# Performance work log

Measured on AMD Instinct MI355X. Metric: run time of the kernel, lower is better.

Reference implementation:

```python
import jax, jax.numpy as jnp
import numpy as np

BS, N, D_IN = 2, 512, 256
HEADS, D_OUT = 8, 64
NEG_SLOPE = 0.2
MASK_VAL = -1000000000.0


def _xavier(key, shape):
    fan_in, fan_out = shape[0], shape[-1]
    limit = float(np.sqrt(6.0 / (fan_in + fan_out)))
    return jax.random.uniform(key, shape, jnp.float32, -limit, limit)


def setup_inputs() -> dict:
    key = jax.random.key(0)
    ks = jax.random.split(key, 6)
    x = jax.random.normal(ks[0], (BS, N, D_IN), jnp.float32)
    adj = jax.random.randint(ks[1], (BS, N, N), 0, 2, jnp.int32)
    # guarantee no fully-masked row (self loops)
    adj = jnp.maximum(adj, jnp.eye(N, dtype=jnp.int32)[None])
    W_src = _xavier(ks[2], (D_IN, HEADS * D_OUT))
    W_tgt = _xavier(ks[3], (D_IN, HEADS * D_OUT))
    W_skip = _xavier(ks[4], (D_IN, HEADS * D_OUT))
    scoring_fn = _xavier(ks[5], (HEADS, D_OUT))
    bias = jnp.zeros((HEADS * D_OUT,), jnp.float32)
    return {"in_nodes_features": x, "adj": adj, "W_src": W_src,
            "W_tgt": W_tgt, "W_skip": W_skip,
            "scoring_fn": scoring_fn, "bias": bias}


def reference(in_nodes_features, adj, W_src, W_tgt, W_skip, scoring_fn, bias):
    x = in_nodes_features
    bs, n, _ = x.shape
    H, d = scoring_fn.shape
    # projections (dropout is identity in eval mode)
    src = (x @ W_src).reshape(bs, n, H, d)  # values & source scores
    tgt = (x @ W_tgt).reshape(bs, n, H, d)
    src_h = jnp.transpose(src, (0, 2, 1, 3))  # (bs,H,n,d)
    tgt_h = jnp.transpose(tgt, (0, 2, 1, 3))  # (bs,H,m,d)
    # GATv2: LeakyReLU(src_i + tgt_j) then dot with scoring vector
    e = jax.nn.leaky_relu(src_h[:, :, :, None, :] + tgt_h[:, :, None, :, :],
                          NEG_SLOPE)              # (bs,H,n,m,d)
    scores = jnp.einsum('hd,bhnmd->bhnm', scoring_fn, e)
    mask = jnp.where(adj[:, None] > 0, 0.0, MASK_VAL)  # (bs,1,n,m)
    attn = jax.nn.softmax(scores + mask, axis=-1)      # (bs,H,n,m)
    out = jnp.einsum('bhnm,bhmd->bhnd', attn, src_h)
    out = jnp.transpose(out, (0, 2, 1, 3))             # (bs,n,H,d)
    # skip connection via skip_proj (dims differ), concat heads, bias, ELU
    out = out + (x @ W_skip).reshape(bs, n, H, d)
    out = out.reshape(bs, n, H * d) + bias
    out = jax.nn.elu(out)
    return out, adj
```

## Files before the change

### kernel.cpp

```cpp
#include <hip/hip_runtime.h>
#include <cstddef>

typedef _Float16 f16;
typedef __attribute__((ext_vector_type(2))) _Float16 f16x2;
typedef __attribute__((ext_vector_type(4))) _Float16 f16x4;
typedef __attribute__((ext_vector_type(8))) _Float16 f16x8;
typedef __attribute__((ext_vector_type(4))) float fx4;

union f16x8u { f16x8 v; f16x2 h[4]; };

#define BS   2
#define NPTS 512
#define DIN  256
#define NH   8
#define DH   64
#define HD   512

__global__ __launch_bounds__(256) void prep_kernel(
    const float* __restrict__ x, const float* __restrict__ W0,
    const float* __restrict__ W1, const float* __restrict__ W2,
    const float* __restrict__ a, const int* __restrict__ adj,
    f16* __restrict__ x16, f16* __restrict__ Wt16, f16* __restrict__ a16,
    float* __restrict__ out_adj)
{
    const int blk = blockIdx.x;
    const int t = threadIdx.x;
    if (blk < 256) {
        int idx = blk * 1024 + t * 4;
        float4 v = *(const float4*)(x + idx);
        f16x4 h = {(f16)v.x, (f16)v.y, (f16)v.z, (f16)v.w};
        *(f16x4*)(x16 + idx) = h;
    } else if (blk < 352) {
        __shared__ float lds[64][65];
        int idx = blk - 256;
        int w = idx >> 5;
        int tile = idx & 31;
        int k0 = (tile >> 3) * 64, n0 = (tile & 7) * 64;
        const float* W = (w == 0) ? W0 : ((w == 1) ? W1 : W2);
        int r = t >> 2;
        int cg = (t & 3) * 16;
        #pragma unroll
        for (int i = 0; i < 4; ++i) {
            float4 v = *(const float4*)(W + (size_t)(k0 + r) * HD + n0 + cg + i * 4);
            lds[r][cg + i * 4 + 0] = v.x;
            lds[r][cg + i * 4 + 1] = v.y;
            lds[r][cg + i * 4 + 2] = v.z;
            lds[r][cg + i * 4 + 3] = v.w;
        }
        __syncthreads();
        f16* dst = Wt16 + (size_t)w * (HD * DIN) + (size_t)(n0 + r) * DIN + k0 + cg;
        #pragma unroll
        for (int i = 0; i < 16; ++i) dst[i] = (f16)lds[cg + i][r];
    } else if (blk == 352) {
        for (int i = t; i < NH * DH; i += 256) a16[i] = (f16)a[i];
    } else {
        int idx = (blk - 353) * 1024 + t * 4;
        int4 v = *(const int4*)(adj + idx);
        float4 fv = {(float)v.x, (float)v.y, (float)v.z, (float)v.w};
        *(float4*)(out_adj + idx) = fv;
    }
}

__global__ __launch_bounds__(256) void proj_kernel(
    const f16* __restrict__ x16, const f16* __restrict__ Wt16,
    f16* __restrict__ src16, f16* __restrict__ srcT16, f16* __restrict__ tgt16,
    float* __restrict__ skipf)
{
    __shared__ f16 Alds[64 * 136];
    __shared__ f16 Blds[64 * 136];
    const int t = threadIdx.x;
    const int mt = blockIdx.x, nt = blockIdx.y, wz = blockIdx.z;
    const f16* Wt = Wt16 + (size_t)wz * (HD * DIN);
    const int lane = t & 63, wv = t >> 6;
    const int l15 = lane & 15, quad = lane >> 4;
    const int moff = (wv & 1) * 32, noff = (wv >> 1) * 32;

    fx4 acc[2][2];
    #pragma unroll
    for (int fi = 0; fi < 2; ++fi)
        #pragma unroll
        for (int fj = 0; fj < 2; ++fj)
            acc[fi][fj] = (fx4){0.f, 0.f, 0.f, 0.f};

    for (int kk = 0; kk < 2; ++kk) {
        if (kk) __syncthreads();
        #pragma unroll
        for (int i = 0; i < 4; ++i) {
            int idx = t + i * 256;
            int row = idx >> 4, seg = idx & 15;
            *(f16x8*)&Alds[row * 136 + seg * 8] =
                *(const f16x8*)(x16 + (size_t)(mt * 64 + row) * DIN + kk * 128 + seg * 8);
            *(f16x8*)&Blds[row * 136 + seg * 8] =
                *(const f16x8*)(Wt + (size_t)(nt * 64 + row) * DIN + kk * 128 + seg * 8);
        }
        __syncthreads();
        #pragma unroll
        for (int ks = 0; ks < 4; ++ks) {
            f16x8 aF[2], bF[2];
            #pragma unroll
            for (int f = 0; f < 2; ++f) {
                aF[f] = *(const f16x8*)&Alds[(moff + f * 16 + l15) * 136 + ks * 32 + quad * 8];
                bF[f] = *(const f16x8*)&Blds[(noff + f * 16 + l15) * 136 + ks * 32 + quad * 8];
            }
            #pragma unroll
            for (int fi = 0; fi < 2; ++fi)
                #pragma unroll
                for (int fj = 0; fj < 2; ++fj)
                    acc[fi][fj] = __builtin_amdgcn_mfma_f32_16x16x32_f16(
                        aF[fi], bF[fj], acc[fi][fj], 0, 0, 0);
        }
    }

    #pragma unroll
    for (int fi = 0; fi < 2; ++fi)
        #pragma unroll
        for (int fj = 0; fj < 2; ++fj)
            #pragma unroll
            for (int i = 0; i < 4; ++i) {
                int rowg = mt * 64 + moff + fi * 16 + quad * 4 + i;
                int colg = nt * 64 + noff + fj * 16 + l15;
                float v = acc[fi][fj][i];
                if (wz == 2) {
                    skipf[(size_t)rowg * HD + colg] = v;
                } else {
                    int bb = rowg >> 9, n = rowg & 511;
                    int hh = colg >> 6, d = colg & 63;
                    size_t bh = (size_t)bb * NH + hh;
                    if (wz == 0) {
                        src16[(bh * NPTS + n) * DH + d] = (f16)v;
                        srcT16[(bh * DH + d) * NPTS + n] = (f16)v;
                    } else {
                        tgt16[(bh * NPTS + n) * DH + d] = (f16)v;
                    }
                }
            }
}

__global__ __launch_bounds__(256) void attn_kernel(
    const f16* __restrict__ src16, const f16* __restrict__ srcT16,
    const f16* __restrict__ tgt16, const f16* __restrict__ a16,
    const float* __restrict__ skipf, const float* __restrict__ bias,
    const int* __restrict__ adj, float* __restrict__ out)
{
    __shared__ f16 tgt_lds[256 * 72];
    __shared__ f16 p_lds[16 * 520];
    __shared__ f16 src_lds[16 * 64];
    __shared__ f16 a_lds[64];

    const int t = threadIdx.x;
    const int lane = t & 63, wv = t >> 6;
    const int n0 = blockIdx.x * 16;
    const int h = blockIdx.y, b = blockIdx.z;
    const int bh = b * NH + h;
    const f16x2 slope2 = {(f16)0.2f, (f16)0.2f};

    if (t < 128) {
        int row = t >> 3, seg = t & 7;
        *(f16x8*)&src_lds[row * 64 + seg * 8] =
            *(const f16x8*)(src16 + ((size_t)bh * NPTS + n0 + row) * DH + seg * 8);
    } else if (t < 136) {
        int seg = t - 128;
        *(f16x8*)&a_lds[seg * 8] = *(const f16x8*)(a16 + h * DH + seg * 8);
    }

    const int r0 = n0 + wv * 4;

    for (int mtile = 0; mtile < 2; ++mtile) {
        __syncthreads();
        #pragma unroll
        for (int i = 0; i < 8; ++i) {
            int idx = t + i * 256;
            int row = idx >> 3, seg = idx & 7;
            *(f16x8*)&tgt_lds[row * 72 + seg * 8] =
                *(const f16x8*)(tgt16 + ((size_t)bh * NPTS + mtile * 256 + row) * DH + seg * 8);
        }
        __syncthreads();

        float sc[4][4] = {{0.f, 0.f, 0.f, 0.f}, {0.f, 0.f, 0.f, 0.f},
                          {0.f, 0.f, 0.f, 0.f}, {0.f, 0.f, 0.f, 0.f}};
        for (int st = 0; st < 8; ++st) {
            f16x8u a8; a8.v = *(const f16x8*)&a_lds[st * 8];
            f16x8u s8[4];
            #pragma unroll
            for (int r = 0; r < 4; ++r)
                s8[r].v = *(const f16x8*)&src_lds[(wv * 4 + r) * 64 + st * 8];
            #pragma unroll
            for (int jj = 0; jj < 4; ++jj) {
                int ml = jj * 64 + lane;
                f16x8u t8; t8.v = *(const f16x8*)&tgt_lds[ml * 72 + st * 8];
                #pragma unroll
                for (int c = 0; c < 4; ++c) {
                    f16x2 t2 = t8.h[c];
                    f16x2 a2 = a8.h[c];
                    #pragma unroll
                    for (int r = 0; r < 4; ++r) {
                        f16x2 z = s8[r].h[c] + t2;
                        f16x2 zl = __builtin_elementwise_max(z, z * slope2);
                        sc[r][jj] = __builtin_amdgcn_fdot2(a2, zl, sc[r][jj], false);
                    }
                }
            }
        }
        #pragma unroll
        for (int r = 0; r < 4; ++r) {
            #pragma unroll
            for (int jj = 0; jj < 4; ++jj) {
                int m = mtile * 256 + jj * 64 + lane;
                int av = adj[((size_t)b * NPTS + r0 + r) * NPTS + m];
                float s = (av > 0) ? sc[r][jj] : -1e30f;
                p_lds[(wv * 4 + r) * 520 + m] = (f16)s;
            }
        }
    }
    __syncthreads();

    #pragma unroll
    for (int r = 0; r < 4; ++r) {
        int row = wv * 4 + r;
        f16x8 v = *(const f16x8*)&p_lds[row * 520 + lane * 8];
        float vf[8];
        #pragma unroll
        for (int i = 0; i < 8; ++i) vf[i] = (float)v[i];
        float mx = vf[0];
        #pragma unroll
        for (int i = 1; i < 8; ++i) mx = fmaxf(mx, vf[i]);
        for (int msk = 1; msk < 64; msk <<= 1) mx = fmaxf(mx, __shfl_xor(mx, msk, 64));
        float l = 0.f;
        #pragma unroll
        for (int i = 0; i < 8; ++i) { vf[i] = __expf(vf[i] - mx); l += vf[i]; }
        for (int msk = 1; msk < 64; msk <<= 1) l += __shfl_xor(l, msk, 64);
        float inv = 1.0f / l;
        f16x8 pv;
        #pragma unroll
        for (int i = 0; i < 8; ++i) pv[i] = (f16)(vf[i] * inv);
        *(f16x8*)&p_lds[row * 520 + lane * 8] = pv;
    }
    __syncthreads();

    const int l15 = lane & 15, quad = lane >> 4;
    fx4 acc = {0.f, 0.f, 0.f, 0.f};
    const f16* vb = srcT16 + ((size_t)bh * DH + wv * 16 + l15) * NPTS;
    #pragma unroll
    for (int ks = 0; ks < 16; ++ks) {
        f16x8 a8 = *(const f16x8*)&p_lds[l15 * 520 + ks * 32 + quad * 8];
        f16x8 b8 = *(const f16x8*)(vb + ks * 32 + quad * 8);
        acc = __builtin_amdgcn_mfma_f32_16x16x32_f16(a8, b8, acc, 0, 0, 0);
    }
    #pragma unroll
    for (int i = 0; i < 4; ++i) {
        int ng = n0 + quad * 4 + i;
        int col = h * DH + wv * 16 + l15;
        size_t oi = ((size_t)b * NPTS + ng) * HD + col;
        float val = acc[i] + skipf[oi] + bias[col];
        out[oi] = (val > 0.f) ? val : __expf(val) - 1.f;
    }
}

extern "C" void kernel_launch(void* const* d_in, const int* in_sizes, int n_in,
                              void* d_out, int out_size, void* d_ws, size_t ws_size,
                              hipStream_t stream) {
    const float* x     = (const float*)d_in[0];
    const int*   adj   = (const int*)d_in[1];
    const float* Wsrc  = (const float*)d_in[2];
    const float* Wtgt  = (const float*)d_in[3];
    const float* Wskip = (const float*)d_in[4];
    const float* a     = (const float*)d_in[5];
    const float* bias  = (const float*)d_in[6];

    float* out = (float*)d_out;
    float* out_adj = out + (size_t)BS * NPTS * NPTS;

    char* wsb = (char*)d_ws;
    f16*   src16  = (f16*)(wsb + 0x000000);
    f16*   srcT16 = (f16*)(wsb + 0x100000);
    f16*   tgt16  = (f16*)(wsb + 0x200000);
    f16*   x16    = (f16*)(wsb + 0x300000);
    f16*   Wt16   = (f16*)(wsb + 0x380000);
    f16*   a16    = (f16*)(wsb + 0x440000);
    float* skipf  = (float*)(wsb + 0x480000);

    prep_kernel<<<865, 256, 0, stream>>>(x, Wsrc, Wtgt, Wskip, a, adj,
                                         x16, Wt16, a16, out_adj);
    proj_kernel<<<dim3(16, 8, 3), 256, 0, stream>>>(x16, Wt16, src16, srcT16,
                                                    tgt16, skipf);
    attn_kernel<<<dim3(32, 8, 2), 256, 0, stream>>>(src16, srcT16, tgt16, a16,
                                                    skipf, bias, adj, out);
}
```

Measured before the change: 103.6 us.

## Fuse fp32-to-fp16 prep into projection GEMM and drop prep kernel launch

Removes the separate prep kernel. The projection kernel now reads fp32 x and W directly, converts them to fp16 while staging into LDS, and transposes W in LDS with scalar stores. The adj-to-float copy moves to extra blocks of the projection kernel, and the attention kernel converts the scoring vector itself. This saves one launch and an intermediate global round trip. In exchange, every GEMM tile re-converts its inputs, and the transposed B writes to LDS may cause bank conflicts.

```diff
diff --git a/kernel.cpp b/kernel.cpp
--- a/kernel.cpp
+++ b/kernel.cpp
@@ -16,63 +16,34 @@
 #define DH   64
 #define HD   512
 
-__global__ __launch_bounds__(256) void prep_kernel(
+__global__ __launch_bounds__(256) void proj_kernel(
     const float* __restrict__ x, const float* __restrict__ W0,
     const float* __restrict__ W1, const float* __restrict__ W2,
-    const float* __restrict__ a, const int* __restrict__ adj,
-    f16* __restrict__ x16, f16* __restrict__ Wt16, f16* __restrict__ a16,
-    float* __restrict__ out_adj)
-{
-    const int blk = blockIdx.x;
-    const int t = threadIdx.x;
-    if (blk < 256) {
-        int idx = blk * 1024 + t * 4;
-        float4 v = *(const float4*)(x + idx);
-        f16x4 h = {(f16)v.x, (f16)v.y, (f16)v.z, (f16)v.w};
-        *(f16x4*)(x16 + idx) = h;
-    } else if (blk < 352) {
-        __shared__ float lds[64][65];
-        int idx = blk - 256;
-        int w = idx >> 5;
-        int tile = idx & 31;
-        int k0 = (tile >> 3) * 64, n0 = (tile & 7) * 64;
-        const float* W = (w == 0) ? W0 : ((w == 1) ? W1 : W2);
-        int r = t >> 2;
-        int cg = (t & 3) * 16;
-        #pragma unroll
-        for (int i = 0; i < 4; ++i) {
-            float4 v = *(const float4*)(W + (size_t)(k0 + r) * HD + n0 + cg + i * 4);
-            lds[r][cg + i * 4 + 0] = v.x;
-            lds[r][cg + i * 4 + 1] = v.y;
-            lds[r][cg + i * 4 + 2] = v.z;
-            lds[r][cg + i * 4 + 3] = v.w;
-        }
-        __syncthreads();
-        f16* dst = Wt16 + (size_t)w * (HD * DIN) + (size_t)(n0 + r) * DIN + k0 + cg;
-        #pragma unroll
-        for (int i = 0; i < 16; ++i) dst[i] = (f16)lds[cg + i][r];
-    } else if (blk == 352) {
-        for (int i = t; i < NH * DH; i += 256) a16[i] = (f16)a[i];
-    } else {
-        int idx = (blk - 353) * 1024 + t * 4;
-        int4 v = *(const int4*)(adj + idx);
-        float4 fv = {(float)v.x, (float)v.y, (float)v.z, (float)v.w};
-        *(float4*)(out_adj + idx) = fv;
-    }
-}
-
-__global__ __launch_bounds__(256) void proj_kernel(
-    const f16* __restrict__ x16, const f16* __restrict__ Wt16,
+    const int* __restrict__ adj,
     f16* __restrict__ src16, f16* __restrict__ srcT16, f16* __restrict__ tgt16,
-    float* __restrict__ skipf)
+    float* __restrict__ skipf, float* __restrict__ out_adj)
 {
     __shared__ f16 Alds[64 * 136];
     __shared__ f16 Blds[64 * 136];
+    const int blk = blockIdx.x;
     const int t = threadIdx.x;
-    const int mt = blockIdx.x, nt = blockIdx.y, wz = blockIdx.z;
-    const f16* Wt = Wt16 + (size_t)wz * (HD * DIN);
     const int lane = t & 63, wv = t >> 6;
     const int l15 = lane & 15, quad = lane >> 4;
+
+    if (blk >= 384) {
+        int id = blk - 384;
+        #pragma unroll
+        for (int j = 0; j < 4; ++j) {
+            int idx = id * 4096 + (t + j * 256) * 4;
+            int4 v = *(const int4*)(adj + idx);
+            float4 fv = {(float)v.x, (float)v.y, (float)v.z, (float)v.w};
+            *(float4*)(out_adj + idx) = fv;
+        }
+        return;
+    }
+
+    const int mt = blk & 15, nt = (blk >> 4) & 7, wz = blk >> 7;
+    const float* W = (wz == 0) ? W0 : ((wz == 1) ? W1 : W2);
     const int moff = (wv & 1) * 32, noff = (wv >> 1) * 32;
 
     fx4 acc[2][2];
@@ -85,13 +56,24 @@
     for (int kk = 0; kk < 2; ++kk) {
         if (kk) __syncthreads();
         #pragma unroll
-        for (int i = 0; i < 4; ++i) {
+        for (int i = 0; i < 8; ++i) {
             int idx = t + i * 256;
-            int row = idx >> 4, seg = idx & 15;
-            *(f16x8*)&Alds[row * 136 + seg * 8] =
-                *(const f16x8*)(x16 + (size_t)(mt * 64 + row) * DIN + kk * 128 + seg * 8);
-            *(f16x8*)&Blds[row * 136 + seg * 8] =
-                *(const f16x8*)(Wt + (size_t)(nt * 64 + row) * DIN + kk * 128 + seg * 8);
+            int row = idx >> 5, c = idx & 31;
+            float4 v = *(const float4*)(x + (size_t)(mt * 64 + row) * DIN
+                                          + kk * 128 + c * 4);
+            f16x4 h = {(f16)v.x, (f16)v.y, (f16)v.z, (f16)v.w};
+            *(f16x4*)&Alds[row * 136 + c * 4] = h;
+        }
+        #pragma unroll
+        for (int i = 0; i < 8; ++i) {
+            int idx = t + i * 256;
+            int k = idx >> 4, c = idx & 15;
+            float4 v = *(const float4*)(W + (size_t)(kk * 128 + k) * HD
+                                          + nt * 64 + c * 4);
+            Blds[(c * 4 + 0) * 136 + k] = (f16)v.x;
+            Blds[(c * 4 + 1) * 136 + k] = (f16)v.y;
+            Blds[(c * 4 + 2) * 136 + k] = (f16)v.z;
+            Blds[(c * 4 + 3) * 136 + k] = (f16)v.w;
         }
         __syncthreads();
         #pragma unroll
@@ -99,8 +81,10 @@
             f16x8 aF[2], bF[2];
             #pragma unroll
             for (int f = 0; f < 2; ++f) {
-                aF[f] = *(const f16x8*)&Alds[(moff + f * 16 + l15) * 136 + ks * 32 + quad * 8];
-                bF[f] = *(const f16x8*)&Blds[(noff + f * 16 + l15) * 136 + ks * 32 + quad * 8];
+                aF[f] = *(const f16x8*)&Alds[(moff + f * 16 + l15) * 136
+                                             + ks * 32 + quad * 8];
+                bF[f] = *(const f16x8*)&Blds[(noff + f * 16 + l15) * 136
+                                             + ks * 32 + quad * 8];
             }
             #pragma unroll
             for (int fi = 0; fi < 2; ++fi)
@@ -138,7 +122,7 @@
 
 __global__ __launch_bounds__(256) void attn_kernel(
     const f16* __restrict__ src16, const f16* __restrict__ srcT16,
-    const f16* __restrict__ tgt16, const f16* __restrict__ a16,
+    const f16* __restrict__ tgt16, const float* __restrict__ a,
     const float* __restrict__ skipf, const float* __restrict__ bias,
     const int* __restrict__ adj, float* __restrict__ out)
 {
@@ -149,8 +133,10 @@
 
     const int t = threadIdx.x;
     const int lane = t & 63, wv = t >> 6;
-    const int n0 = blockIdx.x * 16;
-    const int h = blockIdx.y, b = blockIdx.z;
+    const int blk = blockIdx.x;
+    const int tile = blk & 31;
+    const int h = (blk >> 5) & 7, b = blk >> 8;
+    const int n0 = tile * 16;
     const int bh = b * NH + h;
     const f16x2 slope2 = {(f16)0.2f, (f16)0.2f};
 
@@ -158,9 +144,8 @@
         int row = t >> 3, seg = t & 7;
         *(f16x8*)&src_lds[row * 64 + seg * 8] =
             *(const f16x8*)(src16 + ((size_t)bh * NPTS + n0 + row) * DH + seg * 8);
-    } else if (t < 136) {
-        int seg = t - 128;
-        *(f16x8*)&a_lds[seg * 8] = *(const f16x8*)(a16 + h * DH + seg * 8);
+    } else if (t < 192) {
+        a_lds[t - 128] = (f16)a[h * DH + (t - 128)];
     }
 
     const int r0 = n0 + wv * 4;
@@ -172,7 +157,8 @@
             int idx = t + i * 256;
             int row = idx >> 3, seg = idx & 7;
             *(f16x8*)&tgt_lds[row * 72 + seg * 8] =
-                *(const f16x8*)(tgt16 + ((size_t)bh * NPTS + mtile * 256 + row) * DH + seg * 8);
+                *(const f16x8*)(tgt16 + ((size_t)bh * NPTS + mtile * 256 + row) * DH
+                                + seg * 8);
         }
         __syncthreads();
 
@@ -274,15 +260,10 @@
     f16*   src16  = (f16*)(wsb + 0x000000);
     f16*   srcT16 = (f16*)(wsb + 0x100000);
     f16*   tgt16  = (f16*)(wsb + 0x200000);
-    f16*   x16    = (f16*)(wsb + 0x300000);
-    f16*   Wt16   = (f16*)(wsb + 0x380000);
-    f16*   a16    = (f16*)(wsb + 0x440000);
-    float* skipf  = (float*)(wsb + 0x480000);
-
-    prep_kernel<<<865, 256, 0, stream>>>(x, Wsrc, Wtgt, Wskip, a, adj,
-                                         x16, Wt16, a16, out_adj);
-    proj_kernel<<<dim3(16, 8, 3), 256, 0, stream>>>(x16, Wt16, src16, srcT16,
-                                                    tgt16, skipf);
-    attn_kernel<<<dim3(32, 8, 2), 256, 0, stream>>>(src16, srcT16, tgt16, a16,
-                                                    skipf, bias, adj, out);
+    float* skipf  = (float*)(wsb + 0x300000);
+
+    proj_kernel<<<512, 256, 0, stream>>>(x, Wsrc, Wtgt, Wskip, adj,
+                                         src16, srcT16, tgt16, skipf, out_adj);
+    attn_kernel<<<512, 256, 0, stream>>>(src16, srcT16, tgt16, a,
+                                         skipf, bias, adj, out);
 }
```

Result: no change. 103.8 us (+0.2%).
